# Kernel optimization log

Hardware: AMD Instinct MI355X
Metric: run time of the kernel (lower is better)

Reference implementation:

```python
import jax, jax.numpy as jnp
import numpy as np

N_NODES = 8192
TOP_K = 32


def setup_inputs() -> dict:
    key = jax.random.key(0)
    k1, k2 = jax.random.split(key)
    scores = jax.random.normal(k1, (N_NODES, N_NODES), dtype=jnp.float32)
    # Gumbel(phi, 1).sample() == phi + Gumbel(0, 1) noise; materialize noise here.
    gumbel_noise = jax.random.gumbel(k2, (N_NODES, N_NODES), dtype=jnp.float32)
    tau = jnp.float32(0.5)
    return {"scores": scores, "gumbel_noise": gumbel_noise, "tau": tau, "k": TOP_K}


def reference(scores, gumbel_noise, tau, k):
    phi = scores / tau                      # [N, N]
    gumbels = phi + gumbel_noise            # reparameterized Gumbel(phi, 1) sample
    _, ind = jax.lax.top_k(gumbels, k)      # [N, k] indices along last dim
    rows = jnp.arange(scores.shape[0])[:, None]
    khot = jnp.zeros_like(gumbels).at[rows, ind].set(1.0)  # k-hot mask [N, N]
    soft = jax.nn.softmax(phi, axis=-1)
    # straight-through: forward = khot, gradient flows through softmax
    return khot + soft - jax.lax.stop_gradient(soft)
```

## Files before the change

kernel.cpp:

```cpp
#include <hip/hip_runtime.h>
#include <stdint.h>


namespace {

constexpr int kN = 8192;
constexpr int kThreads = 256;
constexpr int kVPT = kN / (kThreads * 4);
constexpr int kEPT = kN / kThreads;

typedef float f32x4 __attribute__((ext_vector_type(4)));

__device__ __forceinline__ uint32_t f2sortable(float x) {
  uint32_t b = __float_as_uint(x);
  return (b & 0x80000000u) ? ~b : (b | 0x80000000u);
}

__global__ __launch_bounds__(kThreads, 4) void st_topk_khot(
    const float* __restrict__ scores, const float* __restrict__ noise,
    const float* __restrict__ tau_p, const int* __restrict__ k_p,
    float* __restrict__ out) {
  __shared__ uint32_t sdata[kN];
  __shared__ uint32_t hist[kThreads];
  __shared__ uint32_t cum[kThreads + 1];
  __shared__ uint32_t bcast[3];

  const int t = threadIdx.x;
  const size_t row = blockIdx.x;
  const float tau = tau_p[0];
  const uint32_t k = (uint32_t)k_p[0];

  const float4* s4 = reinterpret_cast<const float4*>(scores + row * (size_t)kN);
  const float4* g4 = reinterpret_cast<const float4*>(noise + row * (size_t)kN);
  uint4* sd4 = reinterpret_cast<uint4*>(sdata);

  uint32_t u[kEPT];

#pragma unroll
  for (int i = 0; i < kVPT; ++i) {
    const int vi = i * kThreads + t;
    float4 s = s4[vi];
    float4 g = g4[vi];
    uint4 q;
    q.x = f2sortable(s.x / tau + g.x);
    q.y = f2sortable(s.y / tau + g.y);
    q.z = f2sortable(s.z / tau + g.z);
    q.w = f2sortable(s.w / tau + g.w);
    u[i * 4 + 0] = q.x;
    u[i * 4 + 1] = q.y;
    u[i * 4 + 2] = q.z;
    u[i * 4 + 3] = q.w;
    sd4[vi] = q;
  }

  uint32_t prefix = 0, pmask = 0, desired = k, eq = 0;

#pragma unroll
  for (int pass = 0; pass < 4; ++pass) {
    const int shift = 24 - pass * 8;
    hist[t] = 0;
    __syncthreads();

    if (pass == 0) {
#pragma unroll
      for (int e = 0; e < kEPT; ++e) {
        const uint32_t b = u[e] >> 24;
        uint64_t m = ~0ull;
#pragma unroll
        for (int bit = 0; bit < 8; ++bit) {
          const uint64_t bal = __ballot((int)((b >> bit) & 1u));
          m &= ((b >> bit) & 1u) ? bal : ~bal;
        }
        if ((threadIdx.x & 63) == __builtin_ctzll(m))
          atomicAdd(&hist[b], (uint32_t)__popcll(m));
      }
    } else {
#pragma unroll
      for (int e = 0; e < kEPT; ++e) {
        if ((u[e] & pmask) == prefix)
          atomicAdd(&hist[(u[e] >> shift) & 255u], 1u);
      }
    }
    __syncthreads();

    cum[t] = hist[t];
    if (t == 0) cum[kThreads] = 0;
#pragma unroll
    for (int off = 1; off < kThreads; off <<= 1) {
      __syncthreads();
      const uint32_t add = (t + off < kThreads) ? cum[t + off] : 0u;
      __syncthreads();
      cum[t] += add;
    }
    __syncthreads();

    const uint32_t cb = cum[t];
    const uint32_t cb1 = cum[t + 1];
    if (cb >= desired && cb1 < desired) {
      bcast[0] = prefix | ((uint32_t)t << shift);
      bcast[1] = desired - cb1;
      bcast[2] = cb - cb1;
    }
    __syncthreads();
    prefix = bcast[0];
    desired = bcast[1];
    eq = bcast[2];
    pmask |= 0xFFu << shift;
    __syncthreads();
  }

  const uint32_t thr = prefix;

  if (eq != desired) {
    if (t == 0) {
      uint32_t need = desired;
      for (int j = 0; j < kN; ++j) {
        if (sdata[j] == thr) {
          if (need) {
            --need;
          } else {
            sdata[j] = 0u;
          }
        }
      }
    }
    __syncthreads();
#pragma unroll
    for (int i = 0; i < kVPT; ++i) {
      uint4 q = sd4[i * kThreads + t];
      u[i * 4 + 0] = q.x;
      u[i * 4 + 1] = q.y;
      u[i * 4 + 2] = q.z;
      u[i * 4 + 3] = q.w;
    }
  }

  f32x4* o4 = reinterpret_cast<f32x4*>(out + row * (size_t)kN);
#pragma unroll
  for (int i = 0; i < kVPT; ++i) {
    const int vi = i * kThreads + t;
    f32x4 o;
    o.x = (u[i * 4 + 0] >= thr) ? 1.0f : 0.0f;
    o.y = (u[i * 4 + 1] >= thr) ? 1.0f : 0.0f;
    o.z = (u[i * 4 + 2] >= thr) ? 1.0f : 0.0f;
    o.w = (u[i * 4 + 3] >= thr) ? 1.0f : 0.0f;
    __builtin_nontemporal_store(o, o4 + vi);
  }
}

}

extern "C" void kernel_launch(void* const* d_in, const int* in_sizes, int n_in,
                              void* d_out, int out_size, void* d_ws, size_t ws_size,
                              hipStream_t stream) {
  (void)in_sizes;
  (void)n_in;
  (void)d_ws;
  (void)ws_size;
  (void)out_size;
  const float* scores = (const float*)d_in[0];
  const float* noise = (const float*)d_in[1];
  const float* tau_p = (const float*)d_in[2];
  const int* k_p = (const int*)d_in[3];
  float* out = (float*)d_out;

  hipLaunchKernelGGL(st_topk_khot, dim3(kN), dim3(kThreads), 0, stream,
                     scores, noise, tau_p, k_p, out);
}
```

Measured before the change: 630.4 us.

## Use single-wavefront rows with ballot-based binary search radix select

Each row is now processed by one 64-lane wavefront holding 128 keys per lane in registers. The shared-memory histogram and prefix-scan passes are replaced by a binary search over thresholds using ballot/popcount counts. Candidates in the top byte bucket are compacted into a small LDS list for the remaining 24-bit search. Ties are resolved in parallel with mbcnt ranks instead of a serial thread-0 scan. The aim is to drop the block barriers and LDS atomics, at the cost of heavy register pressure (128 keys per lane) and lower per-block parallelism.

```diff
diff --git a/kernel.cpp b/kernel.cpp
--- a/kernel.cpp
+++ b/kernel.cpp
@@ -5,9 +5,11 @@
 namespace {
 
 constexpr int kN = 8192;
-constexpr int kThreads = 256;
-constexpr int kVPT = kN / (kThreads * 4);
-constexpr int kEPT = kN / kThreads;
+constexpr int kLanes = 64;
+constexpr int kVPT = kN / (kLanes * 4);
+constexpr int kEPT = kN / kLanes;
+constexpr int kCap = 512;
+constexpr int kLJ = kCap / kLanes;
 
 typedef float f32x4 __attribute__((ext_vector_type(4)));
 
@@ -16,143 +18,203 @@
   return (b & 0x80000000u) ? ~b : (b | 0x80000000u);
 }
 
-__global__ __launch_bounds__(kThreads, 4) void st_topk_khot(
+__device__ __forceinline__ uint32_t mbcnt64(uint64_t m) {
+  return __builtin_amdgcn_mbcnt_hi(
+      (uint32_t)(m >> 32), __builtin_amdgcn_mbcnt_lo((uint32_t)m, 0u));
+}
+
+__global__ __launch_bounds__(kLanes, 3) void st_topk_khot(
     const float* __restrict__ scores, const float* __restrict__ noise,
     const float* __restrict__ tau_p, const int* __restrict__ k_p,
     float* __restrict__ out) {
-  __shared__ uint32_t sdata[kN];
-  __shared__ uint32_t hist[kThreads];
-  __shared__ uint32_t cum[kThreads + 1];
-  __shared__ uint32_t bcast[3];
-
-  const int t = threadIdx.x;
+  __shared__ uint32_t list[kCap];
+
+  const int lane = threadIdx.x;
   const size_t row = blockIdx.x;
+  f32x4* o4 = reinterpret_cast<f32x4*>(out + row * (size_t)kN);
+
+  uint32_t k = (uint32_t)k_p[0];
+  if (k > (uint32_t)kN) k = (uint32_t)kN;
+  if (k == 0u) {
+    f32x4 z = {0.0f, 0.0f, 0.0f, 0.0f};
+#pragma unroll
+    for (int i = 0; i < kVPT; ++i)
+      __builtin_nontemporal_store(z, o4 + i * kLanes + lane);
+    return;
+  }
+
   const float tau = tau_p[0];
-  const uint32_t k = (uint32_t)k_p[0];
-
-  const float4* s4 = reinterpret_cast<const float4*>(scores + row * (size_t)kN);
-  const float4* g4 = reinterpret_cast<const float4*>(noise + row * (size_t)kN);
-  uint4* sd4 = reinterpret_cast<uint4*>(sdata);
+  const f32x4* s4 = reinterpret_cast<const f32x4*>(scores + row * (size_t)kN);
+  const f32x4* g4 = reinterpret_cast<const f32x4*>(noise + row * (size_t)kN);
 
   uint32_t u[kEPT];
+  {
+    const uint32_t tb = __float_as_uint(tau);
+    const uint32_t texp = tb & 0x7F800000u;
+    const bool pow2 =
+        ((tb & 0x807FFFFFu) == 0u) && (texp != 0u) && (texp != 0x7F800000u);
+    if (pow2) {
+      const float r = 1.0f / tau;
+#pragma unroll
+      for (int i = 0; i < kVPT; ++i) {
+        f32x4 s = s4[i * kLanes + lane];
+        f32x4 g = g4[i * kLanes + lane];
+        u[4 * i + 0] = f2sortable(s.x * r + g.x);
+        u[4 * i + 1] = f2sortable(s.y * r + g.y);
+        u[4 * i + 2] = f2sortable(s.z * r + g.z);
+        u[4 * i + 3] = f2sortable(s.w * r + g.w);
+      }
+    } else {
+#pragma unroll
+      for (int i = 0; i < kVPT; ++i) {
+        f32x4 s = s4[i * kLanes + lane];
+        f32x4 g = g4[i * kLanes + lane];
+        u[4 * i + 0] = f2sortable(s.x / tau + g.x);
+        u[4 * i + 1] = f2sortable(s.y / tau + g.y);
+        u[4 * i + 2] = f2sortable(s.z / tau + g.z);
+        u[4 * i + 3] = f2sortable(s.w / tau + g.w);
+      }
+    }
+  }
+
+  auto probe_all = [&](uint32_t X) -> uint32_t {
+    uint32_t c = 0;
+#pragma unroll
+    for (int e = 0; e < kEPT; ++e)
+      c += (uint32_t)__popcll(__ballot(u[e] >= X));
+    return c;
+  };
+
+  uint32_t lo = 0, hi = 256;
+  uint32_t cge = (uint32_t)kN;
+  uint32_t chi = 0;
+  while (hi - lo > 1u) {
+    const uint32_t mid = (lo + hi) >> 1;
+    const uint32_t c = probe_all(mid << 24);
+    if (c >= k) {
+      lo = mid;
+      cge = c;
+    } else {
+      hi = mid;
+      chi = c;
+    }
+  }
+  const uint32_t d0 = lo;
+  const uint32_t pfx = d0 << 24;
+  const uint32_t cin = cge - chi;
+
+  uint32_t T, cgeT, cgtT;
+  if (d0 != 0u && cin <= (uint32_t)kCap) {
+#pragma unroll
+    for (int j = 0; j < kLJ; ++j) list[j * kLanes + lane] = 0u;
+    __syncthreads();
+    uint32_t base = 0;
+#pragma unroll
+    for (int e = 0; e < kEPT; ++e) {
+      const bool act = (u[e] >> 24) == d0;
+      const uint64_t bal = __ballot(act);
+      if (bal) {
+        if (act) list[base + mbcnt64(bal)] = u[e];
+        base += (uint32_t)__popcll(bal);
+      }
+    }
+    __syncthreads();
+    uint32_t lj[kLJ];
+#pragma unroll
+    for (int j = 0; j < kLJ; ++j) lj[j] = list[j * kLanes + lane];
+
+    uint32_t mlo = 0, mhi = 1u << 24;
+    uint32_t clo = cge, cgt = chi;
+    while (mhi - mlo > 1u) {
+      const uint32_t mm = (mlo + mhi) >> 1;
+      const uint32_t X = pfx | mm;
+      uint32_t c = chi;
+#pragma unroll
+      for (int j = 0; j < kLJ; ++j)
+        c += (uint32_t)__popcll(__ballot(lj[j] >= X));
+      if (c >= k) {
+        mlo = mm;
+        clo = c;
+      } else {
+        mhi = mm;
+        cgt = c;
+      }
+    }
+    T = pfx | mlo;
+    cgeT = clo;
+    cgtT = cgt;
+  } else {
+    uint32_t mlo = 0, mhi = 1u << 24;
+    uint32_t clo = cge, cgt = chi;
+    while (mhi - mlo > 1u) {
+      const uint32_t mm = (mlo + mhi) >> 1;
+      const uint32_t c = probe_all(pfx | mm);
+      if (c >= k) {
+        mlo = mm;
+        clo = c;
+      } else {
+        mhi = mm;
+        cgt = c;
+      }
+    }
+    T = pfx | mlo;
+    cgeT = clo;
+    cgtT = cgt;
+  }
+
+  if (cgeT != k) {
+    const uint32_t need = k - cgtT;
+    uint32_t base = 0;
+#pragma unroll
+    for (int i = 0; i < kVPT; ++i) {
+      const uint32_t q0 = u[4 * i + 0], q1 = u[4 * i + 1];
+      const uint32_t q2 = u[4 * i + 2], q3 = u[4 * i + 3];
+      const uint32_t e0 = (q0 == T), e1 = (q1 == T);
+      const uint32_t e2 = (q2 == T), e3 = (q3 == T);
+      const uint64_t b0 = __ballot(e0), b1 = __ballot(e1);
+      const uint64_t b2 = __ballot(e2), b3 = __ballot(e3);
+      uint32_t keep0 = (q0 > T), keep1 = (q1 > T);
+      uint32_t keep2 = (q2 > T), keep3 = (q3 > T);
+      if (b0 | b1 | b2 | b3) {
+        const uint32_t below =
+            mbcnt64(b0) + mbcnt64(b1) + mbcnt64(b2) + mbcnt64(b3);
+        const uint32_t r0 = base + below;
+        const uint32_t r1 = r0 + e0;
+        const uint32_t r2 = r1 + e1;
+        const uint32_t r3 = r2 + e2;
+        keep0 |= (e0 && r0 < need);
+        keep1 |= (e1 && r1 < need);
+        keep2 |= (e2 && r2 < need);
+        keep3 |= (e3 && r3 < need);
+        base += (uint32_t)(__popcll(b0) + __popcll(b1) + __popcll(b2) +
+                           __popcll(b3));
+      }
+      f32x4 o;
+      o.x = keep0 ? 1.0f : 0.0f;
+      o.y = keep1 ? 1.0f : 0.0f;
+      o.z = keep2 ? 1.0f : 0.0f;
+      o.w = keep3 ? 1.0f : 0.0f;
+      __builtin_nontemporal_store(o, o4 + i * kLanes + lane);
+    }
+    return;
+  }
 
 #pragma unroll
   for (int i = 0; i < kVPT; ++i) {
-    const int vi = i * kThreads + t;
-    float4 s = s4[vi];
-    float4 g = g4[vi];
-    uint4 q;
-    q.x = f2sortable(s.x / tau + g.x);
-    q.y = f2sortable(s.y / tau + g.y);
-    q.z = f2sortable(s.z / tau + g.z);
-    q.w = f2sortable(s.w / tau + g.w);
-    u[i * 4 + 0] = q.x;
-    u[i * 4 + 1] = q.y;
-    u[i * 4 + 2] = q.z;
-    u[i * 4 + 3] = q.w;
-    sd4[vi] = q;
-  }
-
-  uint32_t prefix = 0, pmask = 0, desired = k, eq = 0;
-
-#pragma unroll
-  for (int pass = 0; pass < 4; ++pass) {
-    const int shift = 24 - pass * 8;
-    hist[t] = 0;
-    __syncthreads();
-
-    if (pass == 0) {
-#pragma unroll
-      for (int e = 0; e < kEPT; ++e) {
-        const uint32_t b = u[e] >> 24;
-        uint64_t m = ~0ull;
-#pragma unroll
-        for (int bit = 0; bit < 8; ++bit) {
-          const uint64_t bal = __ballot((int)((b >> bit) & 1u));
-          m &= ((b >> bit) & 1u) ? bal : ~bal;
-        }
-        if ((threadIdx.x & 63) == __builtin_ctzll(m))
-          atomicAdd(&hist[b], (uint32_t)__popcll(m));
-      }
-    } else {
-#pragma unroll
-      for (int e = 0; e < kEPT; ++e) {
-        if ((u[e] & pmask) == prefix)
-          atomicAdd(&hist[(u[e] >> shift) & 255u], 1u);
-      }
-    }
-    __syncthreads();
-
-    cum[t] = hist[t];
-    if (t == 0) cum[kThreads] = 0;
-#pragma unroll
-    for (int off = 1; off < kThreads; off <<= 1) {
-      __syncthreads();
-      const uint32_t add = (t + off < kThreads) ? cum[t + off] : 0u;
-      __syncthreads();
-      cum[t] += add;
-    }
-    __syncthreads();
-
-    const uint32_t cb = cum[t];
-    const uint32_t cb1 = cum[t + 1];
-    if (cb >= desired && cb1 < desired) {
-      bcast[0] = prefix | ((uint32_t)t << shift);
-      bcast[1] = desired - cb1;
-      bcast[2] = cb - cb1;
-    }
-    __syncthreads();
-    prefix = bcast[0];
-    desired = bcast[1];
-    eq = bcast[2];
-    pmask |= 0xFFu << shift;
-    __syncthreads();
-  }
-
-  const uint32_t thr = prefix;
-
-  if (eq != desired) {
-    if (t == 0) {
-      uint32_t need = desired;
-      for (int j = 0; j < kN; ++j) {
-        if (sdata[j] == thr) {
-          if (need) {
-            --need;
-          } else {
-            sdata[j] = 0u;
-          }
-        }
-      }
-    }
-    __syncthreads();
-#pragma unroll
-    for (int i = 0; i < kVPT; ++i) {
-      uint4 q = sd4[i * kThreads + t];
-      u[i * 4 + 0] = q.x;
-      u[i * 4 + 1] = q.y;
-      u[i * 4 + 2] = q.z;
-      u[i * 4 + 3] = q.w;
-    }
-  }
-
-  f32x4* o4 = reinterpret_cast<f32x4*>(out + row * (size_t)kN);
-#pragma unroll
-  for (int i = 0; i < kVPT; ++i) {
-    const int vi = i * kThreads + t;
     f32x4 o;
-    o.x = (u[i * 4 + 0] >= thr) ? 1.0f : 0.0f;
-    o.y = (u[i * 4 + 1] >= thr) ? 1.0f : 0.0f;
-    o.z = (u[i * 4 + 2] >= thr) ? 1.0f : 0.0f;
-    o.w = (u[i * 4 + 3] >= thr) ? 1.0f : 0.0f;
-    __builtin_nontemporal_store(o, o4 + vi);
+    o.x = (u[4 * i + 0] >= T) ? 1.0f : 0.0f;
+    o.y = (u[4 * i + 1] >= T) ? 1.0f : 0.0f;
+    o.z = (u[4 * i + 2] >= T) ? 1.0f : 0.0f;
+    o.w = (u[4 * i + 3] >= T) ? 1.0f : 0.0f;
+    __builtin_nontemporal_store(o, o4 + i * kLanes + lane);
   }
 }
 
 }
 
 extern "C" void kernel_launch(void* const* d_in, const int* in_sizes, int n_in,
-                              void* d_out, int out_size, void* d_ws, size_t ws_size,
-                              hipStream_t stream) {
+                              void* d_out, int out_size, void* d_ws,
+                              size_t ws_size, hipStream_t stream) {
   (void)in_sizes;
   (void)n_in;
   (void)d_ws;
@@ -164,6 +226,6 @@
   const int* k_p = (const int*)d_in[3];
   float* out = (float*)d_out;
 
-  hipLaunchKernelGGL(st_topk_khot, dim3(kN), dim3(kThreads), 0, stream,
-                     scores, noise, tau_p, k_p, out);
-}
+  hipLaunchKernelGGL(st_topk_khot, dim3(kN), dim3(kLanes), 0, stream, scores,
+                     noise, tau_p, k_p, out);
+}
```

Result: slower. 689.6 us (+9.4%).
